# Kernel tuning notes

Measured on AMD Instinct MI355X. Metric: run time of the kernel, lower is better.

The kernel has to match this reference:

```python
import jax, jax.numpy as jnp
import numpy as np

B, N, E, C1, C2 = 8, 4096, 2048, 128, 128
DENSITY = 0.05  # incidence matrix sparsity (stored dense, as in the original)


def setup_inputs() -> dict:
    key = jax.random.key(0)
    kx, kh, kw = jax.random.split(key, 3)
    x = jax.random.normal(kx, (B, N, C1), dtype=jnp.float32)
    # binary hypergraph incidence matrix [B, n_node, n_edge]
    H = (jax.random.uniform(kh, (B, N, E)) < DENSITY).astype(jnp.float32)
    W = jax.random.normal(kw, (C1, C2), dtype=jnp.float32) * 0.02
    b = jnp.zeros((C2,), dtype=jnp.float32)
    return {"x": x, "H": H, "W": W, "b": b}


def _mean_agg(path, X):
    # path: [B, T, S], X: [B, S, D] -> mean-aggregated [B, T, D]
    out = jnp.matmul(path, X)
    s = jnp.sum(path, axis=2, keepdims=True)  # [B, T, 1]
    # 1/s with inf (s==0) masked to 0, fused as a single where
    return jnp.where(s > 0, out / s, jnp.zeros_like(out))


def reference(x, H, W, b):
    # fc: [B, N, C1] -> [B, N, C2]
    x = jnp.matmul(x, W) + b
    # v2e: aggregate node features into hyperedge features
    Ht = jnp.swapaxes(H, 1, 2)  # [B, E, N]
    e = _mean_agg(Ht, x)        # [B, E, C2]
    # e2v: aggregate hyperedge features back to nodes
    v = _mean_agg(H, e)         # [B, N, C2]
    return v
```

## Files before the change

### kernel.cpp

```cpp
#include <hip/hip_runtime.h>
#include <stdint.h>

constexpr int B_ = 8, N_ = 4096, E_ = 2048, C_ = 128;
constexpr int KT = 32;
constexpr int MT = 64;
constexpr int NJW = 2;

typedef short bf16x8 __attribute__((ext_vector_type(8)));
typedef float f32x4  __attribute__((ext_vector_type(4)));

__device__ inline uint16_t bf16_rne(float f) {
    uint32_t u = __builtin_bit_cast(uint32_t, f);
    return (uint16_t)((u + 0x7FFFu + ((u >> 16) & 1u)) >> 16);
}

constexpr size_t HT_E  = (size_t)B_ * (N_ / 32) * E_;
constexpr size_t WT_E  = (size_t)C_ * C_;
constexpr size_t EBF_E = (size_t)B_ * C_ * E_;
constexpr size_t RS_E  = (size_t)B_ * E_;
constexpr size_t RD_E  = (size_t)B_ * N_;

__global__ void pack_kernel(const float* __restrict__ H, uint32_t* __restrict__ HT) {
    const int t  = threadIdx.x;
    const int eg = blockIdx.x & 7;
    const int ng = (blockIdx.x >> 3) & 127;
    const int b  = blockIdx.x >> 10;
    const int e  = eg * 256 + t;
    const float* hp = H + ((size_t)b * N_ + ng * 32) * E_ + e;
    uint32_t w = 0;
#pragma unroll
    for (int i = 0; i < 32; ++i) w |= (hp[(size_t)i * E_] > 0.5f) ? (1u << i) : 0u;
    HT[((size_t)b * (N_ / 32) + ng) * E_ + e] = w;
}

__global__ void prep_kernel(const float* __restrict__ W, const uint32_t* __restrict__ HT,
                            uint16_t* __restrict__ WTb, float* __restrict__ rs_e,
                            float* __restrict__ rd_n) {
    const int blk = blockIdx.x, t = threadIdx.x;
    if (blk < 256) {
        const int wave = t >> 6, lane = t & 63;
        const int wid  = blk * 4 + wave;
        const int b = wid >> 7, ng = wid & 127;
        const uint32_t* p = HT + ((size_t)b * (N_ / 32) + ng) * E_;
        int cnt = 0;
#pragma unroll 1
        for (int c8 = 0; c8 < E_ / 64; ++c8) {
            const uint32_t w = p[c8 * 64 + lane];
#pragma unroll
            for (int i = 0; i < 32; ++i) {
                unsigned long long m = __ballot((w >> i) & 1u);
                if (lane == i) cnt += __popcll(m);
            }
        }
        if (lane < 32)
            rd_n[(size_t)b * N_ + ng * 32 + lane] = (cnt > 0) ? 1.f / (float)cnt : 0.f;
    } else if (blk < 320) {
        const int i = (blk - 256) * 256 + t;
        const int b = i >> 11, e = i & 2047;
        const uint32_t* p = HT + (size_t)b * (N_ / 32) * E_ + e;
        int s = 0;
#pragma unroll 1
        for (int ng = 0; ng < N_ / 32; ++ng) s += __popc(p[(size_t)ng * E_]);
        rs_e[i] = (s > 0) ? 1.f / (float)s : 0.f;
    } else {
        const int i = (blk - 320) * 256 + t;
        const int c = i >> 7, k = i & 127;
        WTb[i] = bf16_rne(W[k * C_ + c]);
    }
}


#define LOADA(S, k0_) do {                                                            \
    if constexpr (MODE == 0) {                                                        \
        _Pragma("unroll")                                                             \
        for (int g = 0; g < NG; ++g) {                                                \
            const float* ap = Ax + ((size_t)batch * N_ + m0 + g * 16 + l15) * C_ + (k0_) + quad * 8; \
            const float4 f0 = *(const float4*)ap;                                     \
            const float4 f1 = *(const float4*)(ap + 4);                               \
            af##S[g*8+0]=f0.x; af##S[g*8+1]=f0.y; af##S[g*8+2]=f0.z; af##S[g*8+3]=f0.w; \
            af##S[g*8+4]=f1.x; af##S[g*8+5]=f1.y; af##S[g*8+6]=f1.z; af##S[g*8+7]=f1.w; \
        }                                                                             \
    } else if constexpr (MODE == 1) {                                                 \
        const uint32_t* p = Hp + (size_t)((k0_) >> 5) * E_ + m0 + l15;                \
        _Pragma("unroll")                                                             \
        for (int g = 0; g < NG; ++g) aw##S[g] = p[g * 16];                            \
    } else {                                                                          \
        const uint32_t* p = Hp + (size_t)(m0 >> 5) * E_ + (k0_) + quad * 8;           \
        _Pragma("unroll")                                                             \
        for (int r = 0; r < NG / 2; ++r) {                                            \
            axl##S[r] = *(const uint4*)(p + r * E_);                                  \
            axh##S[r] = *(const uint4*)(p + r * E_ + 4);                              \
        }                                                                             \
    } } while (0)

#define LOADB(S, k0_) do {                                                            \
    _Pragma("unroll")                                                                 \
    for (int j2 = 0; j2 < NJW; ++j2)                                                  \
        bq##S[j2] = *(const bf16x8*)&Bp[(size_t)((jw + j2) * 16 + l15) * K + (k0_) + quad * 8]; \
    } while (0)

#define MKFRAGS(S, A)                                                                 \
    bf16x8 A[NG];                                                                     \
    do {                                                                              \
    if constexpr (MODE == 0) {                                                        \
        _Pragma("unroll")                                                             \
        for (int g = 0; g < NG; ++g)                                                  \
            { _Pragma("unroll")                                                       \
              for (int jj = 0; jj < 8; ++jj) A[g][jj] = (short)bf16_rne(af##S[g*8+jj]); } \
    } else if constexpr (MODE == 1) {                                                 \
        _Pragma("unroll")                                                             \
        for (int g = 0; g < NG; ++g) {                                                \
            const uint32_t w = aw##S[g];                                              \
            _Pragma("unroll")                                                         \
            for (int jj = 0; jj < 8; ++jj)                                            \
                A[g][jj] = (short)(((w >> (quad * 8 + jj)) & 1u) ? 0x3F80 : 0);       \
        }                                                                             \
    } else {                                                                          \
        _Pragma("unroll")                                                             \
        for (int g = 0; g < NG; ++g) {                                                \
            const int row = g >> 1, bit = (g & 1) * 16 + l15;                         \
            const uint32_t u[8] = {axl##S[row].x, axl##S[row].y, axl##S[row].z, axl##S[row].w, \
                                   axh##S[row].x, axh##S[row].y, axh##S[row].z, axh##S[row].w}; \
            _Pragma("unroll")                                                         \
            for (int jj = 0; jj < 8; ++jj)                                            \
                A[g][jj] = (short)(((u[jj] >> bit) & 1u) ? 0x3F80 : 0);               \
        }                                                                             \
    } } while (0)

template <int MODE, int REP>
__device__ __attribute__((always_inline))
void gemm_body(const float* __restrict__ Ax, const uint32_t* __restrict__ HT,
               const uint16_t* __restrict__ Btb, const float* __restrict__ bias,
               const float* __restrict__ rcp, uint16_t* __restrict__ outT,
               float* __restrict__ outF) {
    constexpr int K   = (MODE == 0) ? C_ : (MODE == 1) ? N_ : E_;
    constexpr int SW  = K / KT;
    constexpr int OLD = (MODE == 0) ? N_ : E_;
    constexpr int RL  = (MODE == 1) ? E_ : N_;
    constexpr int NG  = MT / 16;
    static_assert(SW >= 4 && SW % 4 == 0, "pipeline needs SW multiple of 4");

    const int t = threadIdx.x, wave = t >> 6, lane = t & 63;
    const int l15 = lane & 15, quad = lane >> 4;
    const int batch = blockIdx.x & 7;
    const int m0 = (blockIdx.x >> 3) * MT;
    const int jw = wave * NJW;

    const uint16_t* Bp = Btb + (MODE == 0 ? (size_t)0 : (size_t)batch * C_ * K);
    const uint32_t* Hp = HT + (size_t)batch * (N_ / 32) * E_;

    f32x4 acc[NG * NJW];
    float    af0[NG * 8], af1[NG * 8], af2[NG * 8], af3[NG * 8];
    uint32_t aw0[NG], aw1[NG], aw2[NG], aw3[NG];
    uint4    axl0[NG / 2], axh0[NG / 2], axl1[NG / 2], axh1[NG / 2];
    uint4    axl2[NG / 2], axh2[NG / 2], axl3[NG / 2], axh3[NG / 2];
    bf16x8   bq0[NJW], bq1[NJW], bq2[NJW], bq3[NJW];

    auto mfma_all = [&](const bf16x8 (&A)[NG], const bf16x8 (&bv)[NJW])
        __attribute__((always_inline)) {
#pragma unroll
        for (int j2 = 0; j2 < NJW; ++j2)
#pragma unroll
            for (int g = 0; g < NG; ++g)
                acc[g * NJW + j2] = __builtin_amdgcn_mfma_f32_16x16x32_bf16(A[g], bv[j2], acc[g * NJW + j2], 0, 0, 0);
    };

#pragma unroll 1
    for (int rep = 0; rep < REP; ++rep) {
#pragma unroll
        for (int i = 0; i < NG * NJW; ++i) acc[i] = (f32x4){0.f, 0.f, 0.f, 0.f};

        LOADA(0, 0);      LOADB(0, 0);
        LOADA(1, KT);     LOADB(1, KT);
        LOADA(2, 2 * KT); LOADB(2, 2 * KT);
        LOADA(3, 3 * KT); LOADB(3, 3 * KT);

#pragma unroll 1
        for (int s = 0; s < SW - 4; s += 4) {
            { MKFRAGS(0, A0); mfma_all(A0, bq0); LOADA(0, (s + 4) * KT); LOADB(0, (s + 4) * KT); }
            { MKFRAGS(1, A1); mfma_all(A1, bq1); LOADA(1, (s + 5) * KT); LOADB(1, (s + 5) * KT); }
            { MKFRAGS(2, A2); mfma_all(A2, bq2); LOADA(2, (s + 6) * KT); LOADB(2, (s + 6) * KT); }
            { MKFRAGS(3, A3); mfma_all(A3, bq3); LOADA(3, (s + 7) * KT); LOADB(3, (s + 7) * KT); }
        }
        { MKFRAGS(0, A0); mfma_all(A0, bq0); }
        { MKFRAGS(1, A1); mfma_all(A1, bq1); }
        { MKFRAGS(2, A2); mfma_all(A2, bq2); }
        { MKFRAGS(3, A3); mfma_all(A3, bq3); }

        float mul[NG][4];
        if constexpr (MODE != 0) {
#pragma unroll
            for (int g = 0; g < NG; ++g) {
                const float4 rv = *(const float4*)&rcp[(size_t)batch * RL + m0 + g * 16 + quad * 4];
                mul[g][0] = rv.x; mul[g][1] = rv.y; mul[g][2] = rv.z; mul[g][3] = rv.w;
            }
        }
#pragma unroll
        for (int g = 0; g < NG; ++g) {
            const int row = m0 + g * 16 + quad * 4;
            if constexpr (MODE == 2) {
                float* op = outF + ((size_t)batch * N_ + row) * C_;
#pragma unroll
                for (int j2 = 0; j2 < NJW; ++j2) {
                    const int c = (jw + j2) * 16 + l15;
#pragma unroll
                    for (int r = 0; r < 4; ++r) op[(size_t)r * C_ + c] = acc[g * NJW + j2][r] * mul[g][r];
                }
            } else {
#pragma unroll
                for (int j2 = 0; j2 < NJW; ++j2) {
                    const int c = (jw + j2) * 16 + l15;
                    float v0, v1, v2, v3;
                    if constexpr (MODE == 0) {
                        float bb = bias[c];
                        v0 = acc[g * NJW + j2][0] + bb; v1 = acc[g * NJW + j2][1] + bb;
                        v2 = acc[g * NJW + j2][2] + bb; v3 = acc[g * NJW + j2][3] + bb;
                    } else {
                        v0 = acc[g * NJW + j2][0] * mul[g][0]; v1 = acc[g * NJW + j2][1] * mul[g][1];
                        v2 = acc[g * NJW + j2][2] * mul[g][2]; v3 = acc[g * NJW + j2][3] * mul[g][3];
                    }
                    uint32_t q0 = (uint32_t)bf16_rne(v0) | ((uint32_t)bf16_rne(v1) << 16);
                    uint32_t q1 = (uint32_t)bf16_rne(v2) | ((uint32_t)bf16_rne(v3) << 16);
                    uint16_t* op = outT + ((size_t)batch * C_ + c) * OLD + row;
                    *(uint2*)op = make_uint2(q0, q1);
                }
            }
        }
    }
}

__global__ __launch_bounds__(256, 2)
void fc_k(const float* __restrict__ Ax, const uint16_t* __restrict__ Btb,
          const float* __restrict__ bias, uint16_t* __restrict__ outT) {
    gemm_body<0, 1>(Ax, nullptr, Btb, bias, nullptr, outT, nullptr);
}
__global__ __launch_bounds__(256, 2)
void v2e_k(const uint32_t* __restrict__ HT, const uint16_t* __restrict__ Btb,
           const float* __restrict__ rcp, uint16_t* __restrict__ outT) {
    gemm_body<1, 1>(nullptr, HT, Btb, nullptr, rcp, outT, nullptr);
}
__global__ __launch_bounds__(256, 2)
void e2v_k(const uint32_t* __restrict__ HT, const uint16_t* __restrict__ Btb,
           const float* __restrict__ rcp, float* __restrict__ outF) {
    gemm_body<2, 1>(nullptr, HT, Btb, nullptr, rcp, nullptr, outF);
}

extern "C" void kernel_launch(void* const* d_in, const int* in_sizes, int n_in,
                              void* d_out, int out_size, void* d_ws, size_t ws_size,
                              hipStream_t stream) {
    const float* x    = (const float*)d_in[0];
    const float* H    = (const float*)d_in[1];
    const float* W    = (const float*)d_in[2];
    const float* bias = (const float*)d_in[3];
    float* out = (float*)d_out;

    uint32_t* HT   = (uint32_t*)d_ws;
    uint16_t* WTb  = (uint16_t*)(HT + HT_E);
    uint16_t* ebfT = WTb + WT_E;
    float*    rs_e = (float*)(ebfT + EBF_E);
    float*    rd_n = rs_e + RS_E;
    uint16_t* xwbT = (uint16_t*)d_out;

    pack_kernel<<<dim3(8192), dim3(256), 0, stream>>>(H, HT);
    prep_kernel<<<dim3(384), dim3(256), 0, stream>>>(W, HT, WTb, rs_e, rd_n);
    fc_k <<<dim3(8 * (N_ / MT)), dim3(256), 0, stream>>>(x, WTb, bias, xwbT);
    v2e_k<<<dim3(8 * (E_ / MT)), dim3(256), 0, stream>>>(HT, xwbT, rs_e, ebfT);
    e2v_k<<<dim3(8 * (N_ / MT)), dim3(256), 0, stream>>>(HT, ebfT, rd_n, out);
}
```

Baseline: 497.4 us.

## Add edge-major transposed bit layout and cheap bit-to-bf16 expansion

The pack kernel now also writes a second, edge-major bit-packed copy of H, built with ballots. This lets e2v load single 32-bit words per row exactly like v2e, instead of gathering two uint4 rows and extracting bits. Node degrees now come from a simple popcount over that copy, replacing the costly ballot loop in prep. Bit unpacking uses a multiply-and-permute trick that yields bf16 2.0 instead of 1.0, so the reciprocal scales are halved to compensate. The cost is an extra 8MB workspace buffer and more work in the pack kernel.

```diff
diff --git a/kernel.cpp b/kernel.cpp
--- a/kernel.cpp
+++ b/kernel.cpp
@@ -8,19 +8,22 @@
 
 typedef short bf16x8 __attribute__((ext_vector_type(8)));
 typedef float f32x4  __attribute__((ext_vector_type(4)));
+typedef unsigned int u32x4 __attribute__((ext_vector_type(4)));
 
 __device__ inline uint16_t bf16_rne(float f) {
     uint32_t u = __builtin_bit_cast(uint32_t, f);
     return (uint16_t)((u + 0x7FFFu + ((u >> 16) & 1u)) >> 16);
 }
 
-constexpr size_t HT_E  = (size_t)B_ * (N_ / 32) * E_;
+constexpr size_t BIT_B = (size_t)(N_ / 32) * E_;
+constexpr size_t HT_E  = (size_t)B_ * BIT_B;
 constexpr size_t WT_E  = (size_t)C_ * C_;
 constexpr size_t EBF_E = (size_t)B_ * C_ * E_;
 constexpr size_t RS_E  = (size_t)B_ * E_;
 constexpr size_t RD_E  = (size_t)B_ * N_;
 
-__global__ void pack_kernel(const float* __restrict__ H, uint32_t* __restrict__ HT) {
+__global__ void pack_kernel(const float* __restrict__ H, uint32_t* __restrict__ HT,
+                            uint32_t* __restrict__ HTe) {
     const int t  = threadIdx.x;
     const int eg = blockIdx.x & 7;
     const int ng = (blockIdx.x >> 3) & 127;
@@ -31,39 +34,41 @@
 #pragma unroll
     for (int i = 0; i < 32; ++i) w |= (hp[(size_t)i * E_] > 0.5f) ? (1u << i) : 0u;
     HT[((size_t)b * (N_ / 32) + ng) * E_ + e] = w;
+
+    const int lane  = t & 63;
+    const int ebase = eg * 256 + (t >> 6) * 64;
+    uint32_t val = 0;
+#pragma unroll
+    for (int i = 0; i < 32; ++i) {
+        unsigned long long m = __ballot((w >> i) & 1u);
+        uint32_t half = (lane < 32) ? (uint32_t)m : (uint32_t)(m >> 32);
+        if ((lane & 31) == i) val = half;
+    }
+    HTe[((size_t)b * (E_ / 32) + (ebase >> 5) + (lane >> 5)) * N_ + ng * 32 + (lane & 31)] = val;
 }
 
 __global__ void prep_kernel(const float* __restrict__ W, const uint32_t* __restrict__ HT,
-                            uint16_t* __restrict__ WTb, float* __restrict__ rs_e,
-                            float* __restrict__ rd_n) {
+                            const uint32_t* __restrict__ HTe, uint16_t* __restrict__ WTb,
+                            float* __restrict__ rs_e, float* __restrict__ rd_n) {
     const int blk = blockIdx.x, t = threadIdx.x;
-    if (blk < 256) {
-        const int wave = t >> 6, lane = t & 63;
-        const int wid  = blk * 4 + wave;
-        const int b = wid >> 7, ng = wid & 127;
-        const uint32_t* p = HT + ((size_t)b * (N_ / 32) + ng) * E_;
-        int cnt = 0;
+    if (blk < 128) {
+        const int i = blk * 256 + t;
+        const int b = i >> 12, n = i & 4095;
+        const uint32_t* p = HTe + (size_t)b * BIT_B + n;
+        int s = 0;
 #pragma unroll 1
-        for (int c8 = 0; c8 < E_ / 64; ++c8) {
-            const uint32_t w = p[c8 * 64 + lane];
-#pragma unroll
-            for (int i = 0; i < 32; ++i) {
-                unsigned long long m = __ballot((w >> i) & 1u);
-                if (lane == i) cnt += __popcll(m);
-            }
-        }
-        if (lane < 32)
-            rd_n[(size_t)b * N_ + ng * 32 + lane] = (cnt > 0) ? 1.f / (float)cnt : 0.f;
-    } else if (blk < 320) {
-        const int i = (blk - 256) * 256 + t;
+        for (int ew = 0; ew < E_ / 32; ++ew) s += __popc(p[(size_t)ew * N_]);
+        rd_n[i] = (s > 0) ? 0.5f / (float)s : 0.f;
+    } else if (blk < 192) {
+        const int i = (blk - 128) * 256 + t;
         const int b = i >> 11, e = i & 2047;
-        const uint32_t* p = HT + (size_t)b * (N_ / 32) * E_ + e;
+        const uint32_t* p = HT + (size_t)b * BIT_B + e;
         int s = 0;
 #pragma unroll 1
         for (int ng = 0; ng < N_ / 32; ++ng) s += __popc(p[(size_t)ng * E_]);
-        rs_e[i] = (s > 0) ? 1.f / (float)s : 0.f;
-    } else {
-        const int i = (blk - 320) * 256 + t;
+        rs_e[i] = (s > 0) ? 0.5f / (float)s : 0.f;
+    } else if (blk < 256) {
+        const int i = (blk - 192) * 256 + t;
         const int c = i >> 7, k = i & 127;
         WTb[i] = bf16_rne(W[k * C_ + c]);
     }
@@ -80,17 +85,10 @@
             af##S[g*8+0]=f0.x; af##S[g*8+1]=f0.y; af##S[g*8+2]=f0.z; af##S[g*8+3]=f0.w; \
             af##S[g*8+4]=f1.x; af##S[g*8+5]=f1.y; af##S[g*8+6]=f1.z; af##S[g*8+7]=f1.w; \
         }                                                                             \
-    } else if constexpr (MODE == 1) {                                                 \
-        const uint32_t* p = Hp + (size_t)((k0_) >> 5) * E_ + m0 + l15;                \
+    } else {                                                                          \
+        const uint32_t* p = Hp + (size_t)((k0_) >> 5) * RL + m0 + l15;                \
         _Pragma("unroll")                                                             \
         for (int g = 0; g < NG; ++g) aw##S[g] = p[g * 16];                            \
-    } else {                                                                          \
-        const uint32_t* p = Hp + (size_t)(m0 >> 5) * E_ + (k0_) + quad * 8;           \
-        _Pragma("unroll")                                                             \
-        for (int r = 0; r < NG / 2; ++r) {                                            \
-            axl##S[r] = *(const uint4*)(p + r * E_);                                  \
-            axh##S[r] = *(const uint4*)(p + r * E_ + 4);                              \
-        }                                                                             \
     } } while (0)
 
 #define LOADB(S, k0_) do {                                                            \
@@ -107,29 +105,26 @@
         for (int g = 0; g < NG; ++g)                                                  \
             { _Pragma("unroll")                                                       \
               for (int jj = 0; jj < 8; ++jj) A[g][jj] = (short)bf16_rne(af##S[g*8+jj]); } \
-    } else if constexpr (MODE == 1) {                                                 \
+    } else {                                                                          \
+        const int qs = quad * 8;                                                      \
         _Pragma("unroll")                                                             \
         for (int g = 0; g < NG; ++g) {                                                \
-            const uint32_t w = aw##S[g];                                              \
-            _Pragma("unroll")                                                         \
-            for (int jj = 0; jj < 8; ++jj)                                            \
-                A[g][jj] = (short)(((w >> (quad * 8 + jj)) & 1u) ? 0x3F80 : 0);       \
-        }                                                                             \
-    } else {                                                                          \
-        _Pragma("unroll")                                                             \
-        for (int g = 0; g < NG; ++g) {                                                \
-            const int row = g >> 1, bit = (g & 1) * 16 + l15;                         \
-            const uint32_t u[8] = {axl##S[row].x, axl##S[row].y, axl##S[row].z, axl##S[row].w, \
-                                   axh##S[row].x, axh##S[row].y, axh##S[row].z, axh##S[row].w}; \
-            _Pragma("unroll")                                                         \
-            for (int jj = 0; jj < 8; ++jj)                                            \
-                A[g][jj] = (short)(((u[jj] >> bit) & 1u) ? 0x3F80 : 0);               \
+            const uint32_t wv = aw##S[g];                                             \
+            const uint32_t nb0 = (wv >> qs) & 0xFu;                                   \
+            const uint32_t nb1 = (wv >> (qs + 4)) & 0xFu;                             \
+            const uint32_t s0m = ((nb0 * 0x204081u) & 0x01010101u) << 6;              \
+            const uint32_t s1m = ((nb1 * 0x204081u) & 0x01010101u) << 6;              \
+            u32x4 qq = { __builtin_amdgcn_perm(s0m, 0u, 0x05000400u),                 \
+                         __builtin_amdgcn_perm(s0m, 0u, 0x07000600u),                 \
+                         __builtin_amdgcn_perm(s1m, 0u, 0x05000400u),                 \
+                         __builtin_amdgcn_perm(s1m, 0u, 0x07000600u) };               \
+            A[g] = __builtin_bit_cast(bf16x8, qq);                                    \
         }                                                                             \
     } } while (0)
 
-template <int MODE, int REP>
+template <int MODE>
 __device__ __attribute__((always_inline))
-void gemm_body(const float* __restrict__ Ax, const uint32_t* __restrict__ HT,
+void gemm_body(const float* __restrict__ Ax, const uint32_t* __restrict__ bits,
                const uint16_t* __restrict__ Btb, const float* __restrict__ bias,
                const float* __restrict__ rcp, uint16_t* __restrict__ outT,
                float* __restrict__ outF) {
@@ -147,13 +142,11 @@
     const int jw = wave * NJW;
 
     const uint16_t* Bp = Btb + (MODE == 0 ? (size_t)0 : (size_t)batch * C_ * K);
-    const uint32_t* Hp = HT + (size_t)batch * (N_ / 32) * E_;
+    const uint32_t* Hp = bits + (size_t)batch * BIT_B;
 
     f32x4 acc[NG * NJW];
     float    af0[NG * 8], af1[NG * 8], af2[NG * 8], af3[NG * 8];
     uint32_t aw0[NG], aw1[NG], aw2[NG], aw3[NG];
-    uint4    axl0[NG / 2], axh0[NG / 2], axl1[NG / 2], axh1[NG / 2];
-    uint4    axl2[NG / 2], axh2[NG / 2], axl3[NG / 2], axh3[NG / 2];
     bf16x8   bq0[NJW], bq1[NJW], bq2[NJW], bq3[NJW];
 
     auto mfma_all = [&](const bf16x8 (&A)[NG], const bf16x8 (&bv)[NJW])
@@ -165,65 +158,62 @@
                 acc[g * NJW + j2] = __builtin_amdgcn_mfma_f32_16x16x32_bf16(A[g], bv[j2], acc[g * NJW + j2], 0, 0, 0);
     };
 
+#pragma unroll
+    for (int i = 0; i < NG * NJW; ++i) acc[i] = (f32x4){0.f, 0.f, 0.f, 0.f};
+
+    LOADA(0, 0);      LOADB(0, 0);
+    LOADA(1, KT);     LOADB(1, KT);
+    LOADA(2, 2 * KT); LOADB(2, 2 * KT);
+    LOADA(3, 3 * KT); LOADB(3, 3 * KT);
+
 #pragma unroll 1
-    for (int rep = 0; rep < REP; ++rep) {
-#pragma unroll
-        for (int i = 0; i < NG * NJW; ++i) acc[i] = (f32x4){0.f, 0.f, 0.f, 0.f};
-
-        LOADA(0, 0);      LOADB(0, 0);
-        LOADA(1, KT);     LOADB(1, KT);
-        LOADA(2, 2 * KT); LOADB(2, 2 * KT);
-        LOADA(3, 3 * KT); LOADB(3, 3 * KT);
-
-#pragma unroll 1
-        for (int s = 0; s < SW - 4; s += 4) {
-            { MKFRAGS(0, A0); mfma_all(A0, bq0); LOADA(0, (s + 4) * KT); LOADB(0, (s + 4) * KT); }
-            { MKFRAGS(1, A1); mfma_all(A1, bq1); LOADA(1, (s + 5) * KT); LOADB(1, (s + 5) * KT); }
-            { MKFRAGS(2, A2); mfma_all(A2, bq2); LOADA(2, (s + 6) * KT); LOADB(2, (s + 6) * KT); }
-            { MKFRAGS(3, A3); mfma_all(A3, bq3); LOADA(3, (s + 7) * KT); LOADB(3, (s + 7) * KT); }
+    for (int s = 0; s < SW - 4; s += 4) {
+        { MKFRAGS(0, A0); mfma_all(A0, bq0); LOADA(0, (s + 4) * KT); LOADB(0, (s + 4) * KT); }
+        { MKFRAGS(1, A1); mfma_all(A1, bq1); LOADA(1, (s + 5) * KT); LOADB(1, (s + 5) * KT); }
+        { MKFRAGS(2, A2); mfma_all(A2, bq2); LOADA(2, (s + 6) * KT); LOADB(2, (s + 6) * KT); }
+        { MKFRAGS(3, A3); mfma_all(A3, bq3); LOADA(3, (s + 7) * KT); LOADB(3, (s + 7) * KT); }
+    }
+    { MKFRAGS(0, A0); mfma_all(A0, bq0); }
+    { MKFRAGS(1, A1); mfma_all(A1, bq1); }
+    { MKFRAGS(2, A2); mfma_all(A2, bq2); }
+    { MKFRAGS(3, A3); mfma_all(A3, bq3); }
+
+    float mul[NG][4];
+    if constexpr (MODE != 0) {
+#pragma unroll
+        for (int g = 0; g < NG; ++g) {
+            const float4 rv = *(const float4*)&rcp[(size_t)batch * RL + m0 + g * 16 + quad * 4];
+            mul[g][0] = rv.x; mul[g][1] = rv.y; mul[g][2] = rv.z; mul[g][3] = rv.w;
         }
-        { MKFRAGS(0, A0); mfma_all(A0, bq0); }
-        { MKFRAGS(1, A1); mfma_all(A1, bq1); }
-        { MKFRAGS(2, A2); mfma_all(A2, bq2); }
-        { MKFRAGS(3, A3); mfma_all(A3, bq3); }
-
-        float mul[NG][4];
-        if constexpr (MODE != 0) {
-#pragma unroll
-            for (int g = 0; g < NG; ++g) {
-                const float4 rv = *(const float4*)&rcp[(size_t)batch * RL + m0 + g * 16 + quad * 4];
-                mul[g][0] = rv.x; mul[g][1] = rv.y; mul[g][2] = rv.z; mul[g][3] = rv.w;
+    }
+#pragma unroll
+    for (int g = 0; g < NG; ++g) {
+        const int row = m0 + g * 16 + quad * 4;
+        if constexpr (MODE == 2) {
+            float* op = outF + ((size_t)batch * N_ + row) * C_;
+#pragma unroll
+            for (int j2 = 0; j2 < NJW; ++j2) {
+                const int c = (jw + j2) * 16 + l15;
+#pragma unroll
+                for (int r = 0; r < 4; ++r) op[(size_t)r * C_ + c] = acc[g * NJW + j2][r] * mul[g][r];
             }
-        }
-#pragma unroll
-        for (int g = 0; g < NG; ++g) {
-            const int row = m0 + g * 16 + quad * 4;
-            if constexpr (MODE == 2) {
-                float* op = outF + ((size_t)batch * N_ + row) * C_;
-#pragma unroll
-                for (int j2 = 0; j2 < NJW; ++j2) {
-                    const int c = (jw + j2) * 16 + l15;
-#pragma unroll
-                    for (int r = 0; r < 4; ++r) op[(size_t)r * C_ + c] = acc[g * NJW + j2][r] * mul[g][r];
+        } else {
+#pragma unroll
+            for (int j2 = 0; j2 < NJW; ++j2) {
+                const int c = (jw + j2) * 16 + l15;
+                float v0, v1, v2, v3;
+                if constexpr (MODE == 0) {
+                    float bb = bias[c];
+                    v0 = acc[g * NJW + j2][0] + bb; v1 = acc[g * NJW + j2][1] + bb;
+                    v2 = acc[g * NJW + j2][2] + bb; v3 = acc[g * NJW + j2][3] + bb;
+                } else {
+                    v0 = acc[g * NJW + j2][0] * mul[g][0]; v1 = acc[g * NJW + j2][1] * mul[g][1];
+                    v2 = acc[g * NJW + j2][2] * mul[g][2]; v3 = acc[g * NJW + j2][3] * mul[g][3];
                 }
-            } else {
-#pragma unroll
-                for (int j2 = 0; j2 < NJW; ++j2) {
-                    const int c = (jw + j2) * 16 + l15;
-                    float v0, v1, v2, v3;
-                    if constexpr (MODE == 0) {
-                        float bb = bias[c];
-                        v0 = acc[g * NJW + j2][0] + bb; v1 = acc[g * NJW + j2][1] + bb;
-                        v2 = acc[g * NJW + j2][2] + bb; v3 = acc[g * NJW + j2][3] + bb;
-                    } else {
-                        v0 = acc[g * NJW + j2][0] * mul[g][0]; v1 = acc[g * NJW + j2][1] * mul[g][1];
-                        v2 = acc[g * NJW + j2][2] * mul[g][2]; v3 = acc[g * NJW + j2][3] * mul[g][3];
-                    }
-                    uint32_t q0 = (uint32_t)bf16_rne(v0) | ((uint32_t)bf16_rne(v1) << 16);
-                    uint32_t q1 = (uint32_t)bf16_rne(v2) | ((uint32_t)bf16_rne(v3) << 16);
-                    uint16_t* op = outT + ((size_t)batch * C_ + c) * OLD + row;
-                    *(uint2*)op = make_uint2(q0, q1);
-                }
+                uint32_t q0 = (uint32_t)bf16_rne(v0) | ((uint32_t)bf16_rne(v1) << 16);
+                uint32_t q1 = (uint32_t)bf16_rne(v2) | ((uint32_t)bf16_rne(v3) << 16);
+                uint16_t* op = outT + ((size_t)batch * C_ + c) * OLD + row;
+                *(uint2*)op = make_uint2(q0, q1);
             }
         }
     }
@@ -232,17 +222,17 @@
 __global__ __launch_bounds__(256, 2)
 void fc_k(const float* __restrict__ Ax, const uint16_t* __restrict__ Btb,
           const float* __restrict__ bias, uint16_t* __restrict__ outT) {
-    gemm_body<0, 1>(Ax, nullptr, Btb, bias, nullptr, outT, nullptr);
+    gemm_body<0>(Ax, nullptr, Btb, bias, nullptr, outT, nullptr);
 }
 __global__ __launch_bounds__(256, 2)
 void v2e_k(const uint32_t* __restrict__ HT, const uint16_t* __restrict__ Btb,
            const float* __restrict__ rcp, uint16_t* __restrict__ outT) {
-    gemm_body<1, 1>(nullptr, HT, Btb, nullptr, rcp, outT, nullptr);
+    gemm_body<1>(nullptr, HT, Btb, nullptr, rcp, outT, nullptr);
 }
 __global__ __launch_bounds__(256, 2)
-void e2v_k(const uint32_t* __restrict__ HT, const uint16_t* __restrict__ Btb,
+void e2v_k(const uint32_t* __restrict__ HTe, const uint16_t* __restrict__ Btb,
            const float* __restrict__ rcp, float* __restrict__ outF) {
-    gemm_body<2, 1>(nullptr, HT, Btb, nullptr, rcp, nullptr, outF);
+    gemm_body<2>(nullptr, HTe, Btb, nullptr, rcp, nullptr, outF);
 }
 
 extern "C" void kernel_launch(void* const* d_in, const int* in_sizes, int n_in,
@@ -255,15 +245,16 @@
     float* out = (float*)d_out;
 
     uint32_t* HT   = (uint32_t*)d_ws;
-    uint16_t* WTb  = (uint16_t*)(HT + HT_E);
+    uint32_t* HTe  = HT + HT_E;
+    uint16_t* WTb  = (uint16_t*)(HTe + HT_E);
     uint16_t* ebfT = WTb + WT_E;
     float*    rs_e = (float*)(ebfT + EBF_E);
     float*    rd_n = rs_e + RS_E;
     uint16_t* xwbT = (uint16_t*)d_out;
 
-    pack_kernel<<<dim3(8192), dim3(256), 0, stream>>>(H, HT);
-    prep_kernel<<<dim3(384), dim3(256), 0, stream>>>(W, HT, WTb, rs_e, rd_n);
+    pack_kernel<<<dim3(8192), dim3(256), 0, stream>>>(H, HT, HTe);
+    prep_kernel<<<dim3(256), dim3(256), 0, stream>>>(W, HT, HTe, WTb, rs_e, rd_n);
     fc_k <<<dim3(8 * (N_ / MT)), dim3(256), 0, stream>>>(x, WTb, bias, xwbT);
     v2e_k<<<dim3(8 * (E_ / MT)), dim3(256), 0, stream>>>(HT, xwbT, rs_e, ebfT);
-    e2v_k<<<dim3(8 * (N_ / MT)), dim3(256), 0, stream>>>(HT, ebfT, rd_n, out);
-}
+    e2v_k<<<dim3(8 * (N_ / MT)), dim3(256), 0, stream>>>(HTe, ebfT, rd_n, out);
+}
```

Result: faster. 472.3 us (-5.0%).
